# Kernel tuning notes

Measured on AMD Instinct MI355X. Metric: run time of the kernel, lower is better.

## Reference

```python
import jax, jax.numpy as jnp
import numpy as np

N_NODES = 50000
N_EDGES = 800000
F_IN = 128
HEADS = 2
F_OUT = 128  # out_channels == nfeat for the residual


def setup_inputs() -> dict:
    key = jax.random.key(0)
    k_x, k_e, k_u, k_c, k_w, k_b = jax.random.split(key, 6)
    x = jax.random.normal(k_x, (N_NODES, F_IN), dtype=jnp.float32)
    edge_index = jax.random.randint(k_e, (2, N_EDGES), 0, N_NODES, dtype=jnp.int64)
    # FeaStConv params (PyG init: normal(mean=0, std=0.1))
    u = 0.1 * jax.random.normal(k_u, (F_IN, HEADS), dtype=jnp.float32)       # attention proj
    c = 0.1 * jax.random.normal(k_c, (HEADS,), dtype=jnp.float32)            # attention bias
    w = 0.1 * jax.random.normal(k_w, (F_IN, HEADS * F_OUT), dtype=jnp.float32)  # lin weight
    bias = 0.1 * jax.random.normal(k_b, (F_OUT,), dtype=jnp.float32)
    return {"x": x, "edge_index": edge_index, "u": u, "c": c, "w": w, "bias": bias}


def _feast_conv(x, edge_index, u, c, w, bias):
    n = x.shape[0]
    # add self loops (PyG FeaStConv default add_self_loops=True)
    loops = jnp.arange(n, dtype=edge_index.dtype)
    src = jnp.concatenate([edge_index[0], loops])  # j (source / message sender)
    dst = jnp.concatenate([edge_index[1], loops])  # i (target / aggregator)
    e = src.shape[0]
    # per-edge attention over heads: q = softmax(u^T (x_j - x_i) + c)
    xi = x[dst]                                   # [E, F_in]
    xj = x[src]                                   # [E, F_in]
    q = jax.nn.softmax((xj - xi) @ u + c, axis=-1)  # [E, H]
    # per-node linear, then gather per edge
    xw = (x @ w).reshape(n, HEADS, F_OUT)         # [N, H, F_out]
    msg = jnp.einsum('eh,ehf->ef', q, xw[src])    # [E, F_out]
    # mean aggregation at destinations
    agg = jax.ops.segment_sum(msg, dst, num_segments=n)
    cnt = jax.ops.segment_sum(jnp.ones((e,), x.dtype), dst, num_segments=n)
    return agg / jnp.maximum(cnt, 1.0)[:, None] + bias


def reference(x, edge_index, u, c, w, bias):
    # module forward: x + relu(FeaStConv(x, edge_index))
    return x + jax.nn.relu(_feast_conv(x, edge_index, u, c, w, bias))
```

## Files before the change

### kernel.cpp

```cpp
#include <hip/hip_runtime.h>
#include <hip/hip_bf16.h>

constexpr int N_NODES = 50000;
constexpr int N_EDGES = 800000;
constexpr int F_IN    = 128;
constexpr int F_OUT   = 128;
constexpr int HEADS   = 2;
constexpr int WCOLS   = HEADS * F_OUT;
constexpr int WE_ROWS = 272;
constexpr int SEG     = 64;

typedef __attribute__((ext_vector_type(8))) short  bf16x8;
typedef __attribute__((ext_vector_type(4))) float  f32x4;
typedef __attribute__((ext_vector_type(2))) float  f32x2;
typedef __attribute__((ext_vector_type(4))) unsigned int u32x4;

static __device__ __forceinline__ unsigned short f32_to_bf16_bits(float f) {
    unsigned int u = __float_as_uint(f);
    u += 0x7fffu + ((u >> 16) & 1u);
    return (unsigned short)(u >> 16);
}

static __device__ __forceinline__ bf16x8 pack_bf16x8(const f32x4 a, const f32x4 b) {
    u32x4 p;
    asm("v_cvt_pk_bf16_f32 %0, %1, %2" : "=v"(p[0]) : "v"(a[0]), "v"(a[1]));
    asm("v_cvt_pk_bf16_f32 %0, %1, %2" : "=v"(p[1]) : "v"(a[2]), "v"(a[3]));
    asm("v_cvt_pk_bf16_f32 %0, %1, %2" : "=v"(p[2]) : "v"(b[0]), "v"(b[1]));
    asm("v_cvt_pk_bf16_f32 %0, %1, %2" : "=v"(p[3]) : "v"(b[2]), "v"(b[3]));
    return __builtin_bit_cast(bf16x8, p);
}

__global__ __launch_bounds__(256) void wt_cnt_kernel(const float* __restrict__ w,
                                                     const float* __restrict__ u,
                                                     unsigned short* __restrict__ wTe,
                                                     int* __restrict__ cnt) {
    const int tid = blockIdx.x * 256 + threadIdx.x;
    if (tid < WE_ROWS * F_IN) {
        const int r = tid >> 7;
        const int k = tid & 127;
        float v;
        if (r < WCOLS)            v = w[k * WCOLS + r];
        else if (r < WCOLS + 2)   v = u[k * HEADS + (r - WCOLS)];
        else                      v = 0.f;
        wTe[tid] = f32_to_bf16_bits(v);
    }
    if (tid < N_NODES) cnt[tid] = 0;
}

constexpr int RG = 4;

__global__ __launch_bounds__(256) void proj_kernel(const float* __restrict__ x,
                                                   const unsigned short* __restrict__ wTe,
                                                   unsigned char* __restrict__ xwf,
                                                   float2* __restrict__ s_tab) {
    const int lane = threadIdx.x & 63;
    const int wv   = threadIdx.x >> 6;
    const int n0   = blockIdx.x * (16 * RG);
    const int l15  = lane & 15;
    const int kg   = lane >> 4;

    f32x4 acc[RG][4];
    f32x4 acc4[RG];
#pragma unroll
    for (int rg = 0; rg < RG; ++rg) {
        acc4[rg] = (f32x4){0.f, 0.f, 0.f, 0.f};
#pragma unroll
        for (int t = 0; t < 4; ++t) acc[rg][t] = acc4[rg];
    }

#pragma unroll
    for (int ks = 0; ks < 4; ++ks) {
        bf16x8 xf[RG];
#pragma unroll
        for (int rg = 0; rg < RG; ++rg) {
            const int row = min(n0 + rg * 16 + l15, N_NODES - 1);
            const float* xp = x + (size_t)row * F_IN + ks * 32 + kg * 8;
            const f32x4 xa = *(const f32x4*)xp;
            const f32x4 xb = *(const f32x4*)(xp + 4);
            xf[rg] = pack_bf16x8(xa, xb);
        }

        const unsigned short* wbase = wTe + (size_t)(wv * 64 + l15) * F_IN + ks * 32 + kg * 8;
        const bf16x8 wf0 = *(const bf16x8*)(wbase);
        const bf16x8 wf1 = *(const bf16x8*)(wbase + 16 * F_IN);
        const bf16x8 wf2 = *(const bf16x8*)(wbase + 32 * F_IN);
        const bf16x8 wf3 = *(const bf16x8*)(wbase + 48 * F_IN);

#pragma unroll
        for (int rg = 0; rg < RG; ++rg) {
            acc[rg][0] = __builtin_amdgcn_mfma_f32_16x16x32_bf16(wf0, xf[rg], acc[rg][0], 0, 0, 0);
            acc[rg][1] = __builtin_amdgcn_mfma_f32_16x16x32_bf16(wf1, xf[rg], acc[rg][1], 0, 0, 0);
            acc[rg][2] = __builtin_amdgcn_mfma_f32_16x16x32_bf16(wf2, xf[rg], acc[rg][2], 0, 0, 0);
            acc[rg][3] = __builtin_amdgcn_mfma_f32_16x16x32_bf16(wf3, xf[rg], acc[rg][3], 0, 0, 0);
        }
        if (wv == 3) {
            const unsigned short* ubase = wTe + (size_t)(256 + l15) * F_IN + ks * 32 + kg * 8;
            const bf16x8 uf = *(const bf16x8*)(ubase);
#pragma unroll
            for (int rg = 0; rg < RG; ++rg)
                acc4[rg] = __builtin_amdgcn_mfma_f32_16x16x32_bf16(uf, xf[rg], acc4[rg], 0, 0, 0);
        }
    }

#pragma unroll
    for (int rg = 0; rg < RG; ++rg) {
        const int row = n0 + rg * 16 + l15;
        if (row < N_NODES) {
            unsigned char* orow = xwf + (size_t)row * WCOLS + wv * 64 + kg * 4;
#pragma unroll
            for (int t = 0; t < 4; ++t) {
                unsigned int pk = 0;
                pk = __builtin_amdgcn_cvt_pk_fp8_f32(acc[rg][t][0], acc[rg][t][1], pk, false);
                pk = __builtin_amdgcn_cvt_pk_fp8_f32(acc[rg][t][2], acc[rg][t][3], pk, true);
                *(unsigned int*)(orow + t * 16) = pk;
            }
            if (wv == 3 && kg == 0) {
                s_tab[row] = make_float2(acc4[rg][0], acc4[rg][1]);
            }
        }
    }
}

constexpr int EPT    = 4;
constexpr int CHUNK  = 256 * EPT;
constexpr int NCHUNK = (N_EDGES + CHUNK - 1) / CHUNK;
constexpr int NGROUP = 8;
constexpr int DRANGE = N_NODES / NGROUP;

__global__ __launch_bounds__(256) void scatter_kernel(const int* __restrict__ ei,
                                                      const float2* __restrict__ s,
                                                      const float* __restrict__ c,
                                                      int* __restrict__ cnt,
                                                      unsigned int* __restrict__ rec) {
    const int g     = blockIdx.x & (NGROUP - 1);
    const int chunk = blockIdx.x >> 3;
    const int dlo   = g * DRANGE;
    const int dhi   = dlo + DRANGE;
    const int base  = chunk * CHUNK + threadIdx.x;
    const float c0 = c[0], c1 = c[1];

    int  dstv[EPT];
    bool keep[EPT];
#pragma unroll
    for (int k = 0; k < EPT; ++k) {
        const int e = base + k * 256;
        const int ec = (e < N_EDGES) ? e : 0;
        dstv[k] = ei[N_EDGES + ec];
        keep[k] = (e < N_EDGES) && (dstv[k] >= dlo) && (dstv[k] < dhi);
    }
    int pos[EPT], srcv[EPT];
#pragma unroll
    for (int k = 0; k < EPT; ++k) {
        pos[k]  = keep[k] ? atomicAdd(&cnt[dstv[k]], 1) : 0;
        const int e = base + k * 256;
        srcv[k] = keep[k] ? ei[e] : 0;
    }
#pragma unroll
    for (int k = 0; k < EPT; ++k) {
        if (keep[k]) {
            const float2 ss = s[srcv[k]];
            const float2 sd = s[dstv[k]];
            const float l0 = ss.x - sd.x + c0;
            const float l1 = ss.y - sd.y + c1;
            const float m  = fmaxf(l0, l1);
            const float e0 = __expf(l0 - m);
            const float e1 = __expf(l1 - m);
            const float q0 = e0 / (e0 + e1);
            const unsigned int q16 = (unsigned int)(q0 * 65535.0f + 0.5f);
            const int p = min(pos[k], SEG - 1);
            rec[(size_t)dstv[k] * SEG + p] = (q16 << 16) | (unsigned int)srcv[k];
        }
    }
}

#define AGG_SLOT(K, A)                                                        \
    {                                                                         \
        const unsigned int r = rp[j + K];                                     \
        const unsigned int g = *(const unsigned int*)(gb + (size_t)(r & 0xffffu) * WCOLS); \
        const float q = fmaf(qsign, (float)(r >> 16) * (1.0f/65535.0f), qbase);\
        const f32x2 glo = __builtin_amdgcn_cvt_pk_f32_fp8(g, false);          \
        const f32x2 ghi = __builtin_amdgcn_cvt_pk_f32_fp8(g, true);           \
        A.x = fmaf(q, glo[0], A.x);                                           \
        A.y = fmaf(q, glo[1], A.y);                                           \
        A.z = fmaf(q, ghi[0], A.z);                                           \
        A.w = fmaf(q, ghi[1], A.w);                                           \
    }

__global__ __launch_bounds__(256) void agg_kernel(const float* __restrict__ x,
                                                  const float* __restrict__ bias,
                                                  const float* __restrict__ c,
                                                  const unsigned char* __restrict__ xwf,
                                                  const unsigned int* __restrict__ rec,
                                                  const int* __restrict__ cnt,
                                                  float* __restrict__ out) {
    const int lane = threadIdx.x & 63;
    const int half = lane >> 5;
    const int l5   = lane & 31;
    const int n    = blockIdx.x * 4 + (threadIdx.x >> 6);
    if (n >= N_NODES) return;
    const int m_cnt = min(cnt[n], SEG);
    const int deg   = m_cnt + 1;
    const unsigned int* rp = rec + (size_t)n * SEG;

    const float qbase = half ? 1.0f : 0.0f;
    const float qsign = half ? -1.0f : 1.0f;
    const unsigned char* gb = xwf + half * F_OUT + 4 * l5;

    const float c0 = c[0], c1 = c[1];
    const float mm = fmaxf(c0, c1);
    const float se0 = __expf(c0 - mm);
    const float se1 = __expf(c1 - mm);
    const float qs = fmaf(qsign, se0 / (se0 + se1), qbase);
    const unsigned int gsv = *(const unsigned int*)(gb + (size_t)n * WCOLS);
    const f32x2 slo = __builtin_amdgcn_cvt_pk_f32_fp8(gsv, false);
    const f32x2 shi = __builtin_amdgcn_cvt_pk_f32_fp8(gsv, true);
    float4 a0, a1 = {0.f,0.f,0.f,0.f}, a2 = a1, a3 = a1;
    float4 a4 = a1, a5 = a1, a6 = a1, a7 = a1;
    a0.x = qs * slo[0];
    a0.y = qs * slo[1];
    a0.z = qs * shi[0];
    a0.w = qs * shi[1];

    int j = 0;
    for (; j + 8 <= m_cnt; j += 8) {
        AGG_SLOT(0, a0) AGG_SLOT(1, a1) AGG_SLOT(2, a2) AGG_SLOT(3, a3)
        AGG_SLOT(4, a4) AGG_SLOT(5, a5) AGG_SLOT(6, a6) AGG_SLOT(7, a7)
    }
    if (j + 4 <= m_cnt) {
        AGG_SLOT(0, a4) AGG_SLOT(1, a5) AGG_SLOT(2, a6) AGG_SLOT(3, a7)
        j += 4;
    }
    for (; j < m_cnt; ++j) {
        AGG_SLOT(0, a0)
    }
    float4 t;
    t.x = ((a0.x + a1.x) + (a2.x + a3.x)) + ((a4.x + a5.x) + (a6.x + a7.x));
    t.y = ((a0.y + a1.y) + (a2.y + a3.y)) + ((a4.y + a5.y) + (a6.y + a7.y));
    t.z = ((a0.z + a1.z) + (a2.z + a3.z)) + ((a4.z + a5.z) + (a6.z + a7.z));
    t.w = ((a0.w + a1.w) + (a2.w + a3.w)) + ((a4.w + a5.w) + (a6.w + a7.w));
    t.x += __shfl_xor(t.x, 32, 64);
    t.y += __shfl_xor(t.y, 32, 64);
    t.z += __shfl_xor(t.z, 32, 64);
    t.w += __shfl_xor(t.w, 32, 64);
    if (half == 0) {
        const float inv = 1.0f / (float)deg;
        const float4 bv = *(const float4*)(bias + 4 * l5);
        const float4 xv = *(const float4*)(x + (size_t)n * F_IN + 4 * l5);
        float4 r;
        r.x = xv.x + fmaxf(fmaf(t.x, inv, bv.x), 0.f);
        r.y = xv.y + fmaxf(fmaf(t.y, inv, bv.y), 0.f);
        r.z = xv.z + fmaxf(fmaf(t.z, inv, bv.z), 0.f);
        r.w = xv.w + fmaxf(fmaf(t.w, inv, bv.w), 0.f);
        *(float4*)(out + (size_t)n * F_OUT + 4 * l5) = r;
    }
}

extern "C" void kernel_launch(void* const* d_in, const int* in_sizes, int n_in,
                              void* d_out, int out_size, void* d_ws, size_t ws_size,
                              hipStream_t stream) {
    const float* x    = (const float*)d_in[0];
    const int*   ei   = (const int*)  d_in[1];
    const float* u    = (const float*)d_in[2];
    const float* c    = (const float*)d_in[3];
    const float* w    = (const float*)d_in[4];
    const float* bias = (const float*)d_in[5];
    float* out = (float*)d_out;

    char* p = (char*)d_ws;
    unsigned char* xwf = (unsigned char*)p;    p += (size_t)N_NODES * WCOLS;
    float2* s_tab  = (float2*)p;               p += (size_t)N_NODES * sizeof(float2);
    int*    cnt    = (int*)p;                  p += (size_t)N_NODES * sizeof(int);
    unsigned short* wTe = (unsigned short*)p;  p += (size_t)WE_ROWS * F_IN * sizeof(unsigned short);
    unsigned int* rec = (unsigned int*)p;

    wt_cnt_kernel<<<(N_NODES + 255) / 256, 256, 0, stream>>>(w, u, wTe, cnt);

    proj_kernel<<<(N_NODES + 16 * RG - 1) / (16 * RG), 256, 0, stream>>>(x, wTe, xwf, s_tab);

    scatter_kernel<<<NGROUP * NCHUNK, 256, 0, stream>>>(ei, s_tab, c, cnt, rec);

    agg_kernel<<<(N_NODES + 3) / 4, 256, 0, stream>>>(x, bias, c, xwf, rec, cnt, out);
}
```

Baseline: 123.0 us.

## Split attention projection out and co-schedule MFMA projection with edge scatter

The attention scores s = x·u now come from a small warp-reduction kernel in fp32. The bf16 MFMA projection to fp8 xw is merged into the scatter kernel as interleaved blocks (one projection block per eight scatter chunks per XCD group), so compute-bound GEMM work and latency-bound atomic scatter can overlap on the GPU. In exchange, x is read by an extra kernel, and the slot-to-role mapping adds branch divergence across blocks and a mixed register footprint.

```diff
diff --git a/kernel.cpp b/kernel.cpp
--- a/kernel.cpp
+++ b/kernel.cpp
@@ -47,78 +47,22 @@
     if (tid < N_NODES) cnt[tid] = 0;
 }
 
-constexpr int RG = 4;
-
-__global__ __launch_bounds__(256) void proj_kernel(const float* __restrict__ x,
-                                                   const unsigned short* __restrict__ wTe,
-                                                   unsigned char* __restrict__ xwf,
-                                                   float2* __restrict__ s_tab) {
+__global__ __launch_bounds__(256) void sproj_kernel(const float* __restrict__ x,
+                                                    const float* __restrict__ u,
+                                                    float2* __restrict__ s) {
     const int lane = threadIdx.x & 63;
-    const int wv   = threadIdx.x >> 6;
-    const int n0   = blockIdx.x * (16 * RG);
-    const int l15  = lane & 15;
-    const int kg   = lane >> 4;
-
-    f32x4 acc[RG][4];
-    f32x4 acc4[RG];
-#pragma unroll
-    for (int rg = 0; rg < RG; ++rg) {
-        acc4[rg] = (f32x4){0.f, 0.f, 0.f, 0.f};
-#pragma unroll
-        for (int t = 0; t < 4; ++t) acc[rg][t] = acc4[rg];
-    }
-
-#pragma unroll
-    for (int ks = 0; ks < 4; ++ks) {
-        bf16x8 xf[RG];
-#pragma unroll
-        for (int rg = 0; rg < RG; ++rg) {
-            const int row = min(n0 + rg * 16 + l15, N_NODES - 1);
-            const float* xp = x + (size_t)row * F_IN + ks * 32 + kg * 8;
-            const f32x4 xa = *(const f32x4*)xp;
-            const f32x4 xb = *(const f32x4*)(xp + 4);
-            xf[rg] = pack_bf16x8(xa, xb);
-        }
-
-        const unsigned short* wbase = wTe + (size_t)(wv * 64 + l15) * F_IN + ks * 32 + kg * 8;
-        const bf16x8 wf0 = *(const bf16x8*)(wbase);
-        const bf16x8 wf1 = *(const bf16x8*)(wbase + 16 * F_IN);
-        const bf16x8 wf2 = *(const bf16x8*)(wbase + 32 * F_IN);
-        const bf16x8 wf3 = *(const bf16x8*)(wbase + 48 * F_IN);
-
-#pragma unroll
-        for (int rg = 0; rg < RG; ++rg) {
-            acc[rg][0] = __builtin_amdgcn_mfma_f32_16x16x32_bf16(wf0, xf[rg], acc[rg][0], 0, 0, 0);
-            acc[rg][1] = __builtin_amdgcn_mfma_f32_16x16x32_bf16(wf1, xf[rg], acc[rg][1], 0, 0, 0);
-            acc[rg][2] = __builtin_amdgcn_mfma_f32_16x16x32_bf16(wf2, xf[rg], acc[rg][2], 0, 0, 0);
-            acc[rg][3] = __builtin_amdgcn_mfma_f32_16x16x32_bf16(wf3, xf[rg], acc[rg][3], 0, 0, 0);
-        }
-        if (wv == 3) {
-            const unsigned short* ubase = wTe + (size_t)(256 + l15) * F_IN + ks * 32 + kg * 8;
-            const bf16x8 uf = *(const bf16x8*)(ubase);
-#pragma unroll
-            for (int rg = 0; rg < RG; ++rg)
-                acc4[rg] = __builtin_amdgcn_mfma_f32_16x16x32_bf16(uf, xf[rg], acc4[rg], 0, 0, 0);
-        }
-    }
-
-#pragma unroll
-    for (int rg = 0; rg < RG; ++rg) {
-        const int row = n0 + rg * 16 + l15;
-        if (row < N_NODES) {
-            unsigned char* orow = xwf + (size_t)row * WCOLS + wv * 64 + kg * 4;
-#pragma unroll
-            for (int t = 0; t < 4; ++t) {
-                unsigned int pk = 0;
-                pk = __builtin_amdgcn_cvt_pk_fp8_f32(acc[rg][t][0], acc[rg][t][1], pk, false);
-                pk = __builtin_amdgcn_cvt_pk_fp8_f32(acc[rg][t][2], acc[rg][t][3], pk, true);
-                *(unsigned int*)(orow + t * 16) = pk;
-            }
-            if (wv == 3 && kg == 0) {
-                s_tab[row] = make_float2(acc4[rg][0], acc4[rg][1]);
-            }
-        }
-    }
+    const int n    = blockIdx.x * 4 + (threadIdx.x >> 6);
+    if (n >= N_NODES) return;
+    const float2 xv = *(const float2*)(x + (size_t)n * F_IN + 2 * lane);
+    const float4 uv = *(const float4*)(u + 4 * lane);
+    float p0 = xv.x * uv.x + xv.y * uv.z;
+    float p1 = xv.x * uv.y + xv.y * uv.w;
+#pragma unroll
+    for (int off = 1; off < 64; off <<= 1) {
+        p0 += __shfl_xor(p0, off, 64);
+        p1 += __shfl_xor(p1, off, 64);
+    }
+    if (lane == 0) s[n] = make_float2(p0, p1);
 }
 
 constexpr int EPT    = 4;
@@ -126,49 +70,116 @@
 constexpr int NCHUNK = (N_EDGES + CHUNK - 1) / CHUNK;
 constexpr int NGROUP = 8;
 constexpr int DRANGE = N_NODES / NGROUP;
-
-__global__ __launch_bounds__(256) void scatter_kernel(const int* __restrict__ ei,
-                                                      const float2* __restrict__ s,
-                                                      const float* __restrict__ c,
-                                                      int* __restrict__ cnt,
-                                                      unsigned int* __restrict__ rec) {
-    const int g     = blockIdx.x & (NGROUP - 1);
-    const int chunk = blockIdx.x >> 3;
-    const int dlo   = g * DRANGE;
-    const int dhi   = dlo + DRANGE;
-    const int base  = chunk * CHUNK + threadIdx.x;
-    const float c0 = c[0], c1 = c[1];
-
-    int  dstv[EPT];
-    bool keep[EPT];
-#pragma unroll
-    for (int k = 0; k < EPT; ++k) {
-        const int e = base + k * 256;
-        const int ec = (e < N_EDGES) ? e : 0;
-        dstv[k] = ei[N_EDGES + ec];
-        keep[k] = (e < N_EDGES) && (dstv[k] >= dlo) && (dstv[k] < dhi);
-    }
-    int pos[EPT], srcv[EPT];
-#pragma unroll
-    for (int k = 0; k < EPT; ++k) {
-        pos[k]  = keep[k] ? atomicAdd(&cnt[dstv[k]], 1) : 0;
-        const int e = base + k * 256;
-        srcv[k] = keep[k] ? ei[e] : 0;
-    }
-#pragma unroll
-    for (int k = 0; k < EPT; ++k) {
-        if (keep[k]) {
-            const float2 ss = s[srcv[k]];
-            const float2 sd = s[dstv[k]];
-            const float l0 = ss.x - sd.x + c0;
-            const float l1 = ss.y - sd.y + c1;
-            const float m  = fmaxf(l0, l1);
-            const float e0 = __expf(l0 - m);
-            const float e1 = __expf(l1 - m);
-            const float q0 = e0 / (e0 + e1);
-            const unsigned int q16 = (unsigned int)(q0 * 65535.0f + 0.5f);
-            const int p = min(pos[k], SEG - 1);
-            rec[(size_t)dstv[k] * SEG + p] = (q16 << 16) | (unsigned int)srcv[k];
+constexpr int RG     = 4;
+constexpr int PROJ_BLOCKS = (N_NODES + 16 * RG - 1) / (16 * RG);
+constexpr int FUSE_SLOTS  = 882;
+
+__global__ __launch_bounds__(256) void fused_kernel(const int* __restrict__ ei,
+                                                    const float2* __restrict__ s,
+                                                    const float* __restrict__ c,
+                                                    int* __restrict__ cnt,
+                                                    unsigned int* __restrict__ rec,
+                                                    const float* __restrict__ x,
+                                                    const unsigned short* __restrict__ wTe,
+                                                    unsigned char* __restrict__ xwf) {
+    const int xcd  = blockIdx.x & (NGROUP - 1);
+    const int slot = blockIdx.x >> 3;
+    const int q    = slot / 9;
+    const int r    = slot - q * 9;
+
+    if (r < 8) {
+        const int chunk = q * 8 + r;
+        if (chunk >= NCHUNK) return;
+        const int dlo  = xcd * DRANGE;
+        const int dhi  = dlo + DRANGE;
+        const int base = chunk * CHUNK + threadIdx.x;
+        const float c0 = c[0], c1 = c[1];
+
+        int  dstv[EPT];
+        bool keep[EPT];
+#pragma unroll
+        for (int k = 0; k < EPT; ++k) {
+            const int e = base + k * 256;
+            const int ec = (e < N_EDGES) ? e : 0;
+            dstv[k] = ei[N_EDGES + ec];
+            keep[k] = (e < N_EDGES) && (dstv[k] >= dlo) && (dstv[k] < dhi);
+        }
+        int pos[EPT], srcv[EPT];
+#pragma unroll
+        for (int k = 0; k < EPT; ++k) {
+            pos[k]  = keep[k] ? atomicAdd(&cnt[dstv[k]], 1) : 0;
+            const int e = base + k * 256;
+            srcv[k] = keep[k] ? ei[e] : 0;
+        }
+#pragma unroll
+        for (int k = 0; k < EPT; ++k) {
+            if (keep[k]) {
+                const float2 ss = s[srcv[k]];
+                const float2 sd = s[dstv[k]];
+                const float l0 = ss.x - sd.x + c0;
+                const float l1 = ss.y - sd.y + c1;
+                const float m  = fmaxf(l0, l1);
+                const float e0 = __expf(l0 - m);
+                const float e1 = __expf(l1 - m);
+                const float q0 = e0 / (e0 + e1);
+                const unsigned int q16 = (unsigned int)(q0 * 65535.0f + 0.5f);
+                const int p = min(pos[k], SEG - 1);
+                rec[(size_t)dstv[k] * SEG + p] = (q16 << 16) | (unsigned int)srcv[k];
+            }
+        }
+    } else {
+        const int pb = q * 8 + xcd;
+        if (pb >= PROJ_BLOCKS) return;
+        const int lane = threadIdx.x & 63;
+        const int wv   = threadIdx.x >> 6;
+        const int n0   = pb * (16 * RG);
+        const int l15  = lane & 15;
+        const int kg   = lane >> 4;
+
+        f32x4 acc[RG][4];
+#pragma unroll
+        for (int rg = 0; rg < RG; ++rg)
+#pragma unroll
+            for (int t = 0; t < 4; ++t) acc[rg][t] = (f32x4){0.f, 0.f, 0.f, 0.f};
+
+#pragma unroll
+        for (int ks = 0; ks < 4; ++ks) {
+            bf16x8 xf[RG];
+#pragma unroll
+            for (int rg = 0; rg < RG; ++rg) {
+                const int row = min(n0 + rg * 16 + l15, N_NODES - 1);
+                const float* xp = x + (size_t)row * F_IN + ks * 32 + kg * 8;
+                const f32x4 xa = *(const f32x4*)xp;
+                const f32x4 xb = *(const f32x4*)(xp + 4);
+                xf[rg] = pack_bf16x8(xa, xb);
+            }
+            const unsigned short* wbase = wTe + (size_t)(wv * 64 + l15) * F_IN + ks * 32 + kg * 8;
+            const bf16x8 wf0 = *(const bf16x8*)(wbase);
+            const bf16x8 wf1 = *(const bf16x8*)(wbase + 16 * F_IN);
+            const bf16x8 wf2 = *(const bf16x8*)(wbase + 32 * F_IN);
+            const bf16x8 wf3 = *(const bf16x8*)(wbase + 48 * F_IN);
+#pragma unroll
+            for (int rg = 0; rg < RG; ++rg) {
+                acc[rg][0] = __builtin_amdgcn_mfma_f32_16x16x32_bf16(wf0, xf[rg], acc[rg][0], 0, 0, 0);
+                acc[rg][1] = __builtin_amdgcn_mfma_f32_16x16x32_bf16(wf1, xf[rg], acc[rg][1], 0, 0, 0);
+                acc[rg][2] = __builtin_amdgcn_mfma_f32_16x16x32_bf16(wf2, xf[rg], acc[rg][2], 0, 0, 0);
+                acc[rg][3] = __builtin_amdgcn_mfma_f32_16x16x32_bf16(wf3, xf[rg], acc[rg][3], 0, 0, 0);
+            }
+        }
+
+#pragma unroll
+        for (int rg = 0; rg < RG; ++rg) {
+            const int row = n0 + rg * 16 + l15;
+            if (row < N_NODES) {
+                unsigned char* orow = xwf + (size_t)row * WCOLS + wv * 64 + kg * 4;
+#pragma unroll
+                for (int t = 0; t < 4; ++t) {
+                    unsigned int pk = 0;
+                    pk = __builtin_amdgcn_cvt_pk_fp8_f32(acc[rg][t][0], acc[rg][t][1], pk, false);
+                    pk = __builtin_amdgcn_cvt_pk_fp8_f32(acc[rg][t][2], acc[rg][t][3], pk, true);
+                    *(unsigned int*)(orow + t * 16) = pk;
+                }
+            }
         }
     }
 }
@@ -275,9 +286,10 @@
 
     wt_cnt_kernel<<<(N_NODES + 255) / 256, 256, 0, stream>>>(w, u, wTe, cnt);
 
-    proj_kernel<<<(N_NODES + 16 * RG - 1) / (16 * RG), 256, 0, stream>>>(x, wTe, xwf, s_tab);
-
-    scatter_kernel<<<NGROUP * NCHUNK, 256, 0, stream>>>(ei, s_tab, c, cnt, rec);
+    sproj_kernel<<<(N_NODES + 3) / 4, 256, 0, stream>>>(x, u, s_tab);
+
+    fused_kernel<<<NGROUP * FUSE_SLOTS, 256, 0, stream>>>(ei, s_tab, c, cnt, rec,
+                                                          x, wTe, xwf);
 
     agg_kernel<<<(N_NODES + 3) / 4, 256, 0, stream>>>(x, bias, c, xwf, rec, cnt, out);
 }
```

New measurement: 124.9 us. Within noise of the previous version (+1.6%).
